# Kernel optimization log

Hardware: AMD Instinct MI355X
Metric: run time of the kernel (lower is better)

Reference implementation:

```python
import jax, jax.numpy as jnp
import numpy as np

N, M, D = 32768, 8192, 64

def setup_inputs() -> dict:
    key = jax.random.key(0)
    k1, k2, k3 = jax.random.split(key, 3)
    inputx = jax.random.normal(k1, (N, D), dtype=jnp.float32)
    y = jax.random.normal(k2, (M, D), dtype=jnp.float32)
    # psi is initialized to zeros in the module, but use random values so the
    # dual-variable subtraction actually affects the argmin/min.
    psi = jax.random.normal(k3, (M,), dtype=jnp.float32)
    return {"inputx": inputx, "y": y, "psi": psi}

def reference(inputx, y, psi):
    # cxy[i,j] = ||x_i||^2 + ||y_j||^2 - 2 <x_i, y_j>   (squared euclidean cost)
    x2 = jnp.sum(inputx * inputx, axis=1, keepdims=True)          # [N,1]
    y2 = jnp.sum(y * y, axis=1)[None, :]                          # [1,M]
    cxy = x2 + y2 - 2.0 * jnp.matmul(inputx, y.T)                 # [N,M]
    # semi-dual: mean_i min_j (c(x_i,y_j) - psi_j) + mean_j psi_j
    loss = jnp.mean(jnp.min(cxy - psi[None, :], axis=1)) + jnp.mean(psi)
    return loss
```

## Files before the change

### kernel.cpp

```cpp
#include <hip/hip_runtime.h>

#define N_ROWS 32768
#define M_COLS 8192
#define D_DIM  64
#define JC     8
#define BLOCK  256
#define GROUPS 8
#define ROWS_PER_BLOCK 512
#define CHUNK  (M_COLS / JC)
#define TJ     128
#define NTILE  (CHUNK / TJ)

typedef _Float16 v8h __attribute__((ext_vector_type(8)));
typedef _Float16 v4h __attribute__((ext_vector_type(4)));
typedef float    v4f __attribute__((ext_vector_type(4)));

__global__ __launch_bounds__(BLOCK) void prep_kernel(
    const float* __restrict__ y, const float* __restrict__ psi,
    _Float16* __restrict__ yh, float* __restrict__ th, float* __restrict__ out) {
    const int tid = threadIdx.x;
    if (blockIdx.x == 0 && tid == 0) out[0] = 0.f;
    const int j = blockIdx.x * 16 + (tid >> 4);
    const int n = tid & 15;
    const float4 v = *(const float4*)(y + (size_t)j * D_DIM + n * 4);
    float s = v.x * v.x + v.y * v.y + v.z * v.z + v.w * v.w;
    v4h hv = { (_Float16)v.x, (_Float16)v.y, (_Float16)v.z, (_Float16)v.w };
    *(v4h*)(yh + (size_t)j * D_DIM + n * 4) = hv;
#pragma unroll
    for (int m = 1; m < 16; m <<= 1) s += __shfl_xor(s, m, 64);
    if (n == 0) th[j] = 0.5f * (psi[j] - s);
}

__global__ __launch_bounds__(BLOCK) void partial_min_kernel(
    const float* __restrict__ x, const _Float16* __restrict__ yh,
    const float* __restrict__ th, float* __restrict__ part) {
    __shared__ __align__(16) _Float16 sY[2][TJ * D_DIM];
    __shared__ __align__(16) float    sTh[2][TJ];

    const int tid  = threadIdx.x;
    const int lane = tid & 63, wave = tid >> 6;
    const int q = lane >> 4, n = lane & 15;
    const int jc    = blockIdx.y;
    const int jbase = jc * CHUNK;
    const int i_wave = blockIdx.x * ROWS_PER_BLOCK + wave * 128;

    v8h a[GROUPS][2];
#pragma unroll
    for (int g = 0; g < GROUPS; ++g) {
        const float* px = x + (size_t)(i_wave + g * 16 + n) * D_DIM + q * 8;
#pragma unroll
        for (int c = 0; c < 2; ++c) {
            float4 f0 = *(const float4*)(px + c * 32);
            float4 f1 = *(const float4*)(px + c * 32 + 4);
            v8h av = { (_Float16)f0.x, (_Float16)f0.y, (_Float16)f0.z, (_Float16)f0.w,
                       (_Float16)f1.x, (_Float16)f1.y, (_Float16)f1.z, (_Float16)f1.w };
            a[g][c] = av;
        }
    }

    float maxs[GROUPS][4];
#pragma unroll
    for (int g = 0; g < GROUPS; ++g)
#pragma unroll
        for (int r = 0; r < 4; ++r) maxs[g][r] = -INFINITY;

    auto stage = [&](int t, int b) {
#pragma unroll
        for (int k = 0; k < 4; ++k) {
            const int sIdx = (k * 4 + wave) * 64 + lane;
            const int row  = sIdx >> 3;
            const int c    = (sIdx & 7) ^ (row & 7);
            const _Float16* g = yh + (size_t)(jbase + t * TJ + row) * D_DIM + c * 8;
            __builtin_amdgcn_global_load_lds(
                (const __attribute__((address_space(1))) void*)g,
                (__attribute__((address_space(3))) void*)(&sY[b][(size_t)(k * 4 + wave) * 512]),
                16, 0, 0);
        }
        if (wave == 0 && lane < 32) {
            const float* gt_ = th + jbase + t * TJ + lane * 4;
            __builtin_amdgcn_global_load_lds(
                (const __attribute__((address_space(1))) void*)gt_,
                (__attribute__((address_space(3))) void*)(&sTh[b][0]),
                16, 0, 0);
        }
    };

    stage(0, 0);
    __syncthreads();

    const int sl0 = q ^ (n & 7);

    for (int t = 0; t < NTILE; ++t) {
        const int cur = t & 1;
        if (t + 1 < NTILE) stage(t + 1, cur ^ 1);

        const _Float16* buf = &sY[cur][0];
        const float* tbuf = &sTh[cur][0];
#pragma unroll 4
        for (int ss = 0; ss < TJ / 16; ++ss) {
            const v8h b0 = *(const v8h*)(buf + (ss * 16 + n) * 64 + sl0 * 8);
            const v8h b1 = *(const v8h*)(buf + (ss * 16 + n) * 64 + (sl0 ^ 4) * 8);
            const float tv = tbuf[ss * 16 + n];
            const v4f tv4 = { tv, tv, tv, tv };
#pragma unroll
            for (int g = 0; g < GROUPS; ++g) {
                v4f acc = __builtin_amdgcn_mfma_f32_16x16x32_f16(a[g][0], b0, tv4, 0, 0, 0);
                acc     = __builtin_amdgcn_mfma_f32_16x16x32_f16(a[g][1], b1, acc, 0, 0, 0);
#pragma unroll
                for (int r = 0; r < 4; ++r)
                    maxs[g][r] = fmaxf(maxs[g][r], acc[r]);
            }
        }
        __syncthreads();
    }

#pragma unroll
    for (int g = 0; g < GROUPS; ++g) {
#pragma unroll
        for (int r = 0; r < 4; ++r) {
            float v = maxs[g][r];
#pragma unroll
            for (int m = 1; m < 16; m <<= 1)
                v = fmaxf(v, __shfl_xor(v, m, 64));
            if (n == 0)
                part[(size_t)jc * N_ROWS + i_wave + g * 16 + q * 4 + r] = -2.f * v;
        }
    }
}

__global__ __launch_bounds__(BLOCK) void reduce_kernel(
    const float* __restrict__ part, const float* __restrict__ x,
    const float* __restrict__ psi, float* __restrict__ out) {
    const int tid = threadIdx.x;
    const int gt  = blockIdx.x * BLOCK + tid;
    float m = part[gt];
#pragma unroll
    for (int c = 1; c < JC; ++c)
        m = fminf(m, part[(size_t)c * N_ROWS + gt]);
    float s = m;
    const float4* xv = (const float4*)x;
    float x2 = 0.f;
#pragma unroll
    for (int k = 0; k < 16; ++k) {
        float4 v = xv[gt + k * 32768];
        x2 += v.x * v.x + v.y * v.y + v.z * v.z + v.w * v.w;
    }
    s = (s + x2) * (1.f / (float)N_ROWS);
    if (gt < M_COLS) s += psi[gt] * (1.f / (float)M_COLS);
    for (int off = 32; off > 0; off >>= 1) s += __shfl_down(s, off, 64);
    __shared__ float tmp[4];
    if ((tid & 63) == 0) tmp[tid >> 6] = s;
    __syncthreads();
    if (tid == 0) atomicAdd(out, tmp[0] + tmp[1] + tmp[2] + tmp[3]);
}

extern "C" void kernel_launch(void* const* d_in, const int* in_sizes, int n_in,
                              void* d_out, int out_size, void* d_ws, size_t ws_size,
                              hipStream_t stream) {
    const float* x   = (const float*)d_in[0];
    const float* y   = (const float*)d_in[1];
    const float* psi = (const float*)d_in[2];
    float* out = (float*)d_out;

    float* part = (float*)d_ws;
    float* th   = part + (size_t)JC * N_ROWS;
    _Float16* yh = (_Float16*)(th + M_COLS);

    prep_kernel<<<M_COLS / 16, BLOCK, 0, stream>>>(y, psi, yh, th, out);
    partial_min_kernel<<<dim3(N_ROWS / ROWS_PER_BLOCK, JC), BLOCK, 0, stream>>>(x, yh, th, part);
    reduce_kernel<<<N_ROWS / BLOCK, BLOCK, 0, stream>>>(part, x, psi, out);
}
```

Baseline: 106.2 us.

## Use per-wave LDS staging without block barriers and fuse reduction via last-block

Each wave now stages its own copy of the y tile into private LDS buffers and waits with s_waitcnt instead of __syncthreads, shrinking the tile to 64 columns so four per-wave copies fit. This removes block-wide barriers from the main MFMA loop. The separate reduce kernel is folded into the main kernel through an atomic done-counter: the last column-chunk block for each row block performs the min, x-norm and psi reduction. The cost is four times the global-to-LDS traffic for y, more LDS use, and a serialized tail of work in the last-arriving blocks.

```diff
diff --git a/kernel.cpp b/kernel.cpp
--- a/kernel.cpp
+++ b/kernel.cpp
@@ -8,7 +8,7 @@
 #define GROUPS 8
 #define ROWS_PER_BLOCK 512
 #define CHUNK  (M_COLS / JC)
-#define TJ     128
+#define TJ     64
 #define NTILE  (CHUNK / TJ)
 
 typedef _Float16 v8h __attribute__((ext_vector_type(8)));
@@ -17,9 +17,13 @@
 
 __global__ __launch_bounds__(BLOCK) void prep_kernel(
     const float* __restrict__ y, const float* __restrict__ psi,
-    _Float16* __restrict__ yh, float* __restrict__ th, float* __restrict__ out) {
+    _Float16* __restrict__ yh, float* __restrict__ th,
+    float* __restrict__ out, int* __restrict__ done) {
     const int tid = threadIdx.x;
-    if (blockIdx.x == 0 && tid == 0) out[0] = 0.f;
+    if (blockIdx.x == 0) {
+        if (tid < 64) done[tid] = 0;
+        else if (tid == 64) out[0] = 0.f;
+    }
     const int j = blockIdx.x * 16 + (tid >> 4);
     const int n = tid & 15;
     const float4 v = *(const float4*)(y + (size_t)j * D_DIM + n * 4);
@@ -33,16 +37,18 @@
 
 __global__ __launch_bounds__(BLOCK) void partial_min_kernel(
     const float* __restrict__ x, const _Float16* __restrict__ yh,
-    const float* __restrict__ th, float* __restrict__ part) {
-    __shared__ __align__(16) _Float16 sY[2][TJ * D_DIM];
-    __shared__ __align__(16) float    sTh[2][TJ];
+    const float* __restrict__ th, const float* __restrict__ psi,
+    float* __restrict__ part, int* __restrict__ done, float* __restrict__ out) {
+    __shared__ __align__(16) _Float16 sY[4][2][TJ * D_DIM];
+    __shared__ __align__(16) float    sTh[4][2][TJ];
 
     const int tid  = threadIdx.x;
     const int lane = tid & 63, wave = tid >> 6;
     const int q = lane >> 4, n = lane & 15;
+    const int rb    = blockIdx.x;
     const int jc    = blockIdx.y;
     const int jbase = jc * CHUNK;
-    const int i_wave = blockIdx.x * ROWS_PER_BLOCK + wave * 128;
+    const int i_wave = rb * ROWS_PER_BLOCK + wave * 128;
 
     v8h a[GROUPS][2];
 #pragma unroll
@@ -66,37 +72,39 @@
 
     auto stage = [&](int t, int b) {
 #pragma unroll
-        for (int k = 0; k < 4; ++k) {
-            const int sIdx = (k * 4 + wave) * 64 + lane;
+        for (int k = 0; k < 8; ++k) {
+            const int sIdx = k * 64 + lane;
             const int row  = sIdx >> 3;
             const int c    = (sIdx & 7) ^ (row & 7);
             const _Float16* g = yh + (size_t)(jbase + t * TJ + row) * D_DIM + c * 8;
             __builtin_amdgcn_global_load_lds(
                 (const __attribute__((address_space(1))) void*)g,
-                (__attribute__((address_space(3))) void*)(&sY[b][(size_t)(k * 4 + wave) * 512]),
+                (__attribute__((address_space(3))) void*)(&sY[wave][b][(size_t)k * 512]),
                 16, 0, 0);
         }
-        if (wave == 0 && lane < 32) {
+        if (lane < 16) {
             const float* gt_ = th + jbase + t * TJ + lane * 4;
             __builtin_amdgcn_global_load_lds(
                 (const __attribute__((address_space(1))) void*)gt_,
-                (__attribute__((address_space(3))) void*)(&sTh[b][0]),
+                (__attribute__((address_space(3))) void*)(&sTh[wave][b][0]),
                 16, 0, 0);
         }
     };
 
     stage(0, 0);
-    __syncthreads();
+    __builtin_amdgcn_s_waitcnt(0);
+    __builtin_amdgcn_sched_barrier(0);
 
     const int sl0 = q ^ (n & 7);
 
+#pragma unroll 1
     for (int t = 0; t < NTILE; ++t) {
         const int cur = t & 1;
         if (t + 1 < NTILE) stage(t + 1, cur ^ 1);
 
-        const _Float16* buf = &sY[cur][0];
-        const float* tbuf = &sTh[cur][0];
-#pragma unroll 4
+        const _Float16* buf = &sY[wave][cur][0];
+        const float*   tbuf = &sTh[wave][cur][0];
+#pragma unroll
         for (int ss = 0; ss < TJ / 16; ++ss) {
             const v8h b0 = *(const v8h*)(buf + (ss * 16 + n) * 64 + sl0 * 8);
             const v8h b1 = *(const v8h*)(buf + (ss * 16 + n) * 64 + (sl0 ^ 4) * 8);
@@ -111,7 +119,8 @@
                     maxs[g][r] = fmaxf(maxs[g][r], acc[r]);
             }
         }
-        __syncthreads();
+        __builtin_amdgcn_s_waitcnt(0);
+        __builtin_amdgcn_sched_barrier(0);
     }
 
 #pragma unroll
@@ -126,32 +135,39 @@
                 part[(size_t)jc * N_ROWS + i_wave + g * 16 + q * 4 + r] = -2.f * v;
         }
     }
-}
 
-__global__ __launch_bounds__(BLOCK) void reduce_kernel(
-    const float* __restrict__ part, const float* __restrict__ x,
-    const float* __restrict__ psi, float* __restrict__ out) {
-    const int tid = threadIdx.x;
-    const int gt  = blockIdx.x * BLOCK + tid;
-    float m = part[gt];
+    __shared__ int isLast;
+    __threadfence();
+    if (tid == 0) isLast = (atomicAdd(&done[rb], 1) == JC - 1);
+    __syncthreads();
+    if (!isLast) return;
+    __threadfence();
+
+    float s = 0.f;
 #pragma unroll
-    for (int c = 1; c < JC; ++c)
-        m = fminf(m, part[(size_t)c * N_ROWS + gt]);
-    float s = m;
-    const float4* xv = (const float4*)x;
-    float x2 = 0.f;
+    for (int rr = 0; rr < 2; ++rr) {
+        const int i = rb * ROWS_PER_BLOCK + rr * 256 + tid;
+        float m = part[i];
 #pragma unroll
-    for (int k = 0; k < 16; ++k) {
-        float4 v = xv[gt + k * 32768];
-        x2 += v.x * v.x + v.y * v.y + v.z * v.z + v.w * v.w;
+        for (int c = 1; c < JC; ++c)
+            m = fminf(m, part[(size_t)c * N_ROWS + i]);
+        const float4* px = (const float4*)(x + (size_t)i * D_DIM);
+        float x2 = 0.f;
+#pragma unroll
+        for (int k = 0; k < D_DIM / 4; ++k) {
+            float4 v = px[k];
+            x2 += v.x * v.x + v.y * v.y + v.z * v.z + v.w * v.w;
+        }
+        s += m + x2;
     }
-    s = (s + x2) * (1.f / (float)N_ROWS);
-    if (gt < M_COLS) s += psi[gt] * (1.f / (float)M_COLS);
+    s *= (1.f / (float)N_ROWS);
+    if (tid < CHUNK / JC)
+        s += psi[rb * 128 + tid] * (1.f / (float)M_COLS);
     for (int off = 32; off > 0; off >>= 1) s += __shfl_down(s, off, 64);
-    __shared__ float tmp[4];
-    if ((tid & 63) == 0) tmp[tid >> 6] = s;
+    __shared__ float red[4];
+    if (lane == 0) red[wave] = s;
     __syncthreads();
-    if (tid == 0) atomicAdd(out, tmp[0] + tmp[1] + tmp[2] + tmp[3]);
+    if (tid == 0) atomicAdd(out, red[0] + red[1] + red[2] + red[3]);
 }
 
 extern "C" void kernel_launch(void* const* d_in, const int* in_sizes, int n_in,
@@ -165,8 +181,9 @@
     float* part = (float*)d_ws;
     float* th   = part + (size_t)JC * N_ROWS;
     _Float16* yh = (_Float16*)(th + M_COLS);
+    int* done = (int*)(yh + (size_t)M_COLS * D_DIM);
 
-    prep_kernel<<<M_COLS / 16, BLOCK, 0, stream>>>(y, psi, yh, th, out);
-    partial_min_kernel<<<dim3(N_ROWS / ROWS_PER_BLOCK, JC), BLOCK, 0, stream>>>(x, yh, th, part);
-    reduce_kernel<<<N_ROWS / BLOCK, BLOCK, 0, stream>>>(part, x, psi, out);
+    prep_kernel<<<M_COLS / 16, BLOCK, 0, stream>>>(y, psi, yh, th, out, done);
+    partial_min_kernel<<<dim3(N_ROWS / ROWS_PER_BLOCK, JC), BLOCK, 0, stream>>>(
+        x, yh, th, psi, part, done, out);
 }
```

New measurement: 149.9 us. +41.1%, slower.
